# Performance work log

Hardware: AMD Instinct MI355X
Metric: run time of the kernel (lower is better)

## Reference

```python
import jax, jax.numpy as jnp
import numpy as np

DIM = 2048
N_HEADS = 32
N_KV_HEADS = 8
HEAD_DIM = DIM // N_HEADS
B, T = 2, 2048


def setup_inputs() -> dict:
    key = jax.random.key(0)
    ks = jax.random.split(key, 5)
    std = 0.02
    return {
        "x": jax.random.normal(ks[0], (B, T, DIM), dtype=jnp.float32),
        "wq": jax.random.normal(ks[1], (DIM, DIM), dtype=jnp.float32) * std,
        "wk": jax.random.normal(ks[2], (N_KV_HEADS * HEAD_DIM, DIM), dtype=jnp.float32) * std,
        "wv": jax.random.normal(ks[3], (N_KV_HEADS * HEAD_DIM, DIM), dtype=jnp.float32) * std,
        "wo": jax.random.normal(ks[4], (DIM, DIM), dtype=jnp.float32) * std,
    }


def _rope_tables(seq_len, head_dim, dtype):
    inv_freq = 1.0 / (10000.0 ** (jnp.arange(0, head_dim, 2, dtype=jnp.float32) / head_dim))
    t = jnp.arange(seq_len, dtype=jnp.float32)
    freqs = jnp.einsum("i,j->ij", t, inv_freq)          # [T, hd/2]
    emb = jnp.concatenate([freqs, freqs], axis=-1)       # [T, hd]
    return jnp.cos(emb).astype(dtype), jnp.sin(emb).astype(dtype)


def _rotate_half(x):
    h = x.shape[-1] // 2
    return jnp.concatenate([-x[..., h:], x[..., :h]], axis=-1)


def reference(x, wq, wk, wv, wo):
    Bc, Tc, C = x.shape
    q = (x @ wq.T).reshape(Bc, Tc, N_HEADS, HEAD_DIM).transpose(0, 2, 1, 3)      # [B,H,T,hd]
    k = (x @ wk.T).reshape(Bc, Tc, N_KV_HEADS, HEAD_DIM).transpose(0, 2, 1, 3)   # [B,Hk,T,hd]
    v = (x @ wv.T).reshape(Bc, Tc, N_KV_HEADS, HEAD_DIM).transpose(0, 2, 1, 3)

    cos, sin = _rope_tables(Tc, HEAD_DIM, x.dtype)  # [T,hd] broadcast over B,H
    q = q * cos + _rotate_half(q) * sin
    k = k * cos + _rotate_half(k) * sin

    rep = N_HEADS // N_KV_HEADS
    k = jnp.repeat(k, rep, axis=1)  # [B,H,T,hd]
    v = jnp.repeat(v, rep, axis=1)

    scale = 1.0 / np.sqrt(HEAD_DIM)
    scores = jnp.einsum("bhqd,bhkd->bhqk", q, k) * scale   # [B,H,T,T]
    causal = jnp.triu(jnp.ones((Tc, Tc), dtype=bool), k=1)
    scores = jnp.where(causal, jnp.asarray(-jnp.inf, scores.dtype), scores)
    attn = jax.nn.softmax(scores, axis=-1)
    out = jnp.einsum("bhqk,bhkd->bhqd", attn, v)           # [B,H,T,hd]
    out = out.transpose(0, 2, 1, 3).reshape(Bc, Tc, C)
    return out @ wo.T
```

## Files before the change

### kernel.cpp

```cpp
#include <hip/hip_runtime.h>


typedef unsigned short u16;
typedef __attribute__((ext_vector_type(8))) short bf16x8;
typedef __attribute__((ext_vector_type(4))) float f32x4;
typedef __attribute__((ext_vector_type(4))) unsigned short u16x4;

constexpr int T_SEQ = 2048;
constexpr int DIMC  = 2048;
constexpr int NHEAD = 32;
constexpr int HDIM  = 64;
constexpr int KVDIM = 512;
constexpr int BATCH = 2;

__device__ __forceinline__ u16 f2bf(float f) {
    union { float f; unsigned int i; } v; v.f = f;
    unsigned int r = v.i + 0x7FFFu + ((v.i >> 16) & 1u);
    return (u16)(r >> 16);
}

__device__ __forceinline__ unsigned int pack2_bf16(float e0, float e1) {
    return __builtin_amdgcn_perm(__float_as_uint(e1), __float_as_uint(e0),
                                 0x07060302u);
}

typedef __attribute__((address_space(1))) unsigned int as1_uint;
typedef __attribute__((address_space(3))) unsigned int as3_uint;
__device__ __forceinline__ void glds16(const u16* g, u16* l) {
    __builtin_amdgcn_global_load_lds((as1_uint*)(u16*)g, (as3_uint*)l, 16, 0, 0);
}

__global__ __launch_bounds__(256) void cvt5(const float* __restrict__ x,
                                            const float* __restrict__ wq,
                                            const float* __restrict__ wk,
                                            const float* __restrict__ wv,
                                            const float* __restrict__ wo,
                                            u16* __restrict__ xb,  u16* __restrict__ wqb,
                                            u16* __restrict__ wkb, u16* __restrict__ wvb,
                                            u16* __restrict__ wob) {
    constexpr int E0 = BATCH * T_SEQ * DIMC;
    constexpr int E1 = E0 + DIMC * DIMC;
    constexpr int E2 = E1 + KVDIM * DIMC;
    constexpr int E3 = E2 + KVDIM * DIMC;
    constexpr int E4 = E3 + DIMC * DIMC;
    for (int i = (blockIdx.x * 256 + threadIdx.x) * 4; i < E4; i += gridDim.x * 1024) {
        const float* s; u16* d; int off;
        if (i < E0)      { s = x;  d = xb;  off = 0;  }
        else if (i < E1) { s = wq; d = wqb; off = E0; }
        else if (i < E2) { s = wk; d = wkb; off = E1; }
        else if (i < E3) { s = wv; d = wvb; off = E2; }
        else             { s = wo; d = wob; off = E3; }
        f32x4 v = *(const f32x4*)(s + (i - off));
        u16x4 o;
        #pragma unroll
        for (int e = 0; e < 4; ++e) o[e] = f2bf(v[e]);
        *(u16x4*)(d + (i - off)) = o;
    }
}

template <bool OUTF32>
__device__ __forceinline__ void dgemm_core(const u16* __restrict__ A,
                                           const u16* __restrict__ W,
                                           void* __restrict__ Cv,
                                           int rowBase, int colBase,
                                           int N, int K, bool rope) {
    __shared__ __align__(16) u16 Ash[2][128 * 64];
    __shared__ __align__(16) u16 Bsh[2][128 * 64];

    const int tid  = threadIdx.x;
    const int lane = tid & 63;
    const int w    = tid >> 6;
    const int quad = lane >> 4;
    const int ln   = lane & 15;
    const int wm   = (w >> 1) * 64;
    const int wn   = (w & 1) * 64;

    const int sr = lane >> 3;
    const int sc = 8 * ((lane & 7) ^ sr);
    const u16* aS = A + (size_t)(rowBase + w * 8 + sr) * K + sc;
    const u16* bS = W + (size_t)(colBase + w * 8 + sr) * K + sc;

    f32x4 acc[4][4] = {};
    const int NT = K / 64;
    const int swz = (ln & 7) * 8;

    #pragma unroll
    for (int r = 0; r < 4; ++r) {
        glds16(aS + (size_t)(r * 32) * K, &Ash[0][(w + 4 * r) * 512]);
        glds16(bS + (size_t)(r * 32) * K, &Bsh[0][(w + 4 * r) * 512]);
    }

    for (int t = 0; t < NT; ++t) {
        const int cb = t & 1;
        __builtin_amdgcn_s_barrier();
        __builtin_amdgcn_sched_barrier(0);

        if (t + 1 < NT) {
            const size_t ko = (size_t)(t + 1) * 64;
            u16* An = &Ash[cb ^ 1][0];
            u16* Bn = &Bsh[cb ^ 1][0];
            #pragma unroll
            for (int r = 0; r < 4; ++r) {
                glds16(aS + ko + (size_t)(r * 32) * K, An + (w + 4 * r) * 512);
                glds16(bS + ko + (size_t)(r * 32) * K, Bn + (w + 4 * r) * 512);
            }
            __builtin_amdgcn_sched_barrier(0);
            __asm__ __volatile__("s_waitcnt vmcnt(8)" ::: "memory");
        } else {
            __asm__ __volatile__("s_waitcnt vmcnt(0)" ::: "memory");
        }
        __builtin_amdgcn_sched_barrier(0);
        __builtin_amdgcn_s_barrier();

        const u16* Ap = &Ash[cb][0];
        const u16* Bp = &Bsh[cb][0];
        #pragma unroll
        for (int q2 = 0; q2 < 2; ++q2) {
            bf16x8 bwf[4];
            #pragma unroll
            for (int n = 0; n < 4; ++n)
                bwf[n] = *(const bf16x8*)(Bp + (wn + n * 16 + ln) * 64
                                             + ((q2 * 32 + quad * 8) ^ swz));
            __builtin_amdgcn_s_setprio(1);
            #pragma unroll
            for (int m = 0; m < 4; ++m) {
                bf16x8 af = *(const bf16x8*)(Ap + (wm + m * 16 + ln) * 64
                                                + ((q2 * 32 + quad * 8) ^ swz));
                #pragma unroll
                for (int n = 0; n < 4; ++n)
                    acc[m][n] = __builtin_amdgcn_mfma_f32_16x16x32_bf16(af, bwf[n], acc[m][n], 0, 0, 0);
            }
            __builtin_amdgcn_s_setprio(0);
        }
    }

    if (rope) {
        #pragma unroll
        for (int j = 0; j < 2; ++j) {
            const int d = j * 16 + ln;
            const float invrev = exp2f(-(float)d * (13.287712379549449f / 32.0f))
                                 * 0.15915494309189535f;
            #pragma unroll
            for (int i = 0; i < 4; ++i) {
                #pragma unroll
                for (int r = 0; r < 4; ++r) {
                    const int t = (rowBase + wm + i * 16 + quad * 4 + r) & (T_SEQ - 1);
                    float rev = (float)t * invrev;
                    float fr = rev - floorf(rev);
                    float sn = __builtin_amdgcn_sinf(fr);
                    float cs = __builtin_amdgcn_cosf(fr);
                    float a0 = acc[i][j][r], a2 = acc[i][j + 2][r];
                    acc[i][j][r]     = a0 * cs - a2 * sn;
                    acc[i][j + 2][r] = a2 * cs + a0 * sn;
                }
            }
        }
    }

    #pragma unroll
    for (int i = 0; i < 4; ++i) {
        int mrow = rowBase + wm + i * 16 + quad * 4;
        #pragma unroll
        for (int j = 0; j < 4; ++j) {
            int n = colBase + wn + j * 16 + ln;
            #pragma unroll
            for (int r = 0; r < 4; ++r) {
                if constexpr (OUTF32)
                    ((float*)Cv)[(size_t)(mrow + r) * N + n] = acc[i][j][r];
                else
                    ((u16*)Cv)[(size_t)(mrow + r) * N + n] = f2bf(acc[i][j][r]);
            }
        }
    }
}

__global__ __launch_bounds__(256, 2) void qkv_gemm(const u16* __restrict__ xb,
                                                   const u16* __restrict__ wqb,
                                                   const u16* __restrict__ wkb,
                                                   const u16* __restrict__ wvb,
                                                   u16* __restrict__ Qb,
                                                   u16* __restrict__ Kb,
                                                   u16* __restrict__ Vb) {
    const int flat = blockIdx.y * 24 + blockIdx.x;
    const int xcd  = flat & 7;
    const int idx  = flat >> 3;
    const int row  = (xcd >> 2) * 16 + idx / 6;
    const int ct   = (xcd & 3) * 6 + idx % 6;
    const int rowBase = row * 128;

    const u16* W; u16* C; int colBase, N; bool rope;
    if (ct < 16)      { W = wqb; C = Qb; colBase = ct * 128;        N = DIMC;  rope = true; }
    else if (ct < 20) { W = wkb; C = Kb; colBase = (ct - 16) * 128; N = KVDIM; rope = true; }
    else              { W = wvb; C = Vb; colBase = (ct - 20) * 128; N = KVDIM; rope = false; }
    dgemm_core<false>(xb, W, C, rowBase, colBase, N, DIMC, rope);
}

__global__ __launch_bounds__(256, 2) void gemm_out(const u16* __restrict__ A,
                                                   const u16* __restrict__ W,
                                                   float* __restrict__ C) {
    const int flat = blockIdx.y * 16 + blockIdx.x;
    const int xcd  = flat & 7;
    const int idx  = flat >> 3;
    const int row  = (xcd >> 2) * 16 + (idx >> 2);
    const int col  = (xcd & 3) * 4 + (idx & 3);
    dgemm_core<true>(A, W, C, row * 128, col * 128, DIMC, DIMC, false);
}

__global__ __launch_bounds__(256) void transpose_v(const u16* __restrict__ V,
                                                   u16* __restrict__ Vt) {
    __shared__ __align__(16) u16 tile[32][33];
    const int x = threadIdx.x & 31;
    const int y = threadIdx.x >> 5;
    const int tok0 = blockIdx.y * 32;
    const int c0   = blockIdx.x * 32;
    #pragma unroll
    for (int yy = 0; yy < 32; yy += 8)
        tile[y + yy][x] = V[(size_t)(tok0 + y + yy) * KVDIM + c0 + x];
    __syncthreads();
    const int b  = tok0 >> 11;
    const int t0 = tok0 & (T_SEQ - 1);
    #pragma unroll
    for (int yy = 0; yy < 32; yy += 8)
        Vt[(size_t)(b * KVDIM + c0 + y + yy) * T_SEQ + t0 + x] = tile[x][y + yy];
}

__global__ __launch_bounds__(256) void attn(const u16* __restrict__ Q,
                                            const u16* __restrict__ Kx,
                                            const u16* __restrict__ Vt,
                                            u16* __restrict__ O) {
    __shared__ __align__(16) u16 Ks[2][64][72];
    __shared__ __align__(16) u16 Vs[2][64][72];

    const int tid  = threadIdx.x;
    const int lane = tid & 63;
    const int w    = tid >> 6;
    const int quad = lane >> 4;
    const int ln   = lane & 15;
    const int h    = blockIdx.y;
    const int b    = blockIdx.z;
    const int kvh  = h >> 2;

    const int srow = tid >> 2;
    const int c    = tid & 3;
    const int scol = c * 16;
    const int vsb  = 32 * (c >> 1) + 4 * (c & 1);
    const u16* kbase = Kx + (size_t)(b * T_SEQ + srow) * KVDIM + kvh * HDIM + scol;
    const u16* vbase = Vt + (size_t)(b * KVDIM + kvh * HDIM + srow) * T_SEQ;

    const float K1 = 0.125f * 1.4426950408889634f;
    const float K2 = 8.0f * 1.4426950408889634f;

    #pragma unroll
    for (int phase = 0; phase < 2; ++phase) {
        const int qt = phase ? (15 - (int)blockIdx.x) : (int)blockIdx.x;
        const int qr0 = qt * 128 + w * 16;

        const u16* qp0 = Q + (size_t)(b * T_SEQ + qr0 + ln) * DIMC + h * HDIM + quad * 8;
        const u16* qp1 = qp0 + (size_t)64 * DIMC;
        const bf16x8 bq00 = *(const bf16x8*)qp0;
        const bf16x8 bq01 = *(const bf16x8*)(qp0 + 32);
        const bf16x8 bq10 = *(const bf16x8*)qp1;
        const bf16x8 bq11 = *(const bf16x8*)(qp1 + 32);

        f32x4 o0[4] = {}, o1[4] = {};
        float ls0 = 0.0f, ls1 = 0.0f;

        bf16x8 kra = *(const bf16x8*)kbase;
        bf16x8 krb = *(const bf16x8*)(kbase + 8);
        bf16x8 vra = *(const bf16x8*)(vbase + scol);
        bf16x8 vrb = *(const bf16x8*)(vbase + scol + 8);

        const int NTk = 2 * qt + 2;
        for (int kt = 0; kt < NTk; ++kt) {
            const int cb = kt & 1;

            *(bf16x8*)&Ks[cb][srow][scol]     = kra;
            *(bf16x8*)&Ks[cb][srow][scol + 8] = krb;
            {
                union { bf16x8 v; u16x4 h4[2]; } ua, ub;
                ua.v = vra; ub.v = vrb;
                *(u16x4*)&Vs[cb][srow][vsb]      = ua.h4[0];
                *(u16x4*)&Vs[cb][srow][vsb + 8]  = ua.h4[1];
                *(u16x4*)&Vs[cb][srow][vsb + 16] = ub.h4[0];
                *(u16x4*)&Vs[cb][srow][vsb + 24] = ub.h4[1];
            }

            if (kt + 1 < NTk) {
                const size_t ko = (size_t)(kt + 1) * 64;
                kra = *(const bf16x8*)(kbase + ko * KVDIM);
                krb = *(const bf16x8*)(kbase + ko * KVDIM + 8);
                vra = *(const bf16x8*)(vbase + ko + scol);
                vrb = *(const bf16x8*)(vbase + ko + scol + 8);
            }

            __asm__ __volatile__("s_waitcnt lgkmcnt(0)" ::: "memory");
            __builtin_amdgcn_s_barrier();

            f32x4 s0[4], s1[4];
            __builtin_amdgcn_s_setprio(1);
            #pragma unroll
            for (int st = 0; st < 4; ++st) {
                bf16x8 kfa = *(const bf16x8*)&Ks[cb][st * 16 + ln][quad * 8];
                bf16x8 kfb = *(const bf16x8*)&Ks[cb][st * 16 + ln][32 + quad * 8];
                f32x4 z0 = {}, z1 = {};
                s0[st] = __builtin_amdgcn_mfma_f32_16x16x32_bf16(kfa, bq00, z0, 0, 0, 0);
                s1[st] = __builtin_amdgcn_mfma_f32_16x16x32_bf16(kfa, bq10, z1, 0, 0, 0);
                s0[st] = __builtin_amdgcn_mfma_f32_16x16x32_bf16(kfb, bq01, s0[st], 0, 0, 0);
                s1[st] = __builtin_amdgcn_mfma_f32_16x16x32_bf16(kfb, bq11, s1[st], 0, 0, 0);
            }
            __builtin_amdgcn_s_setprio(0);

            unsigned int pk0[8], pk1[8];
            #pragma unroll
            for (int g = 0; g < 2; ++g) {
                const f32x4* s = g ? s1 : s0;
                unsigned int* pk = g ? pk1 : pk0;
                float lsum = 0.0f;
                const int kdiff = kt - (2 * qt + g);
                if (kdiff < 0) {
                    #pragma unroll
                    for (int st = 0; st < 4; ++st) {
                        float e0 = exp2f(fmaf(s[st][0], K1, -K2));
                        float e1 = exp2f(fmaf(s[st][1], K1, -K2));
                        float e2 = exp2f(fmaf(s[st][2], K1, -K2));
                        float e3 = exp2f(fmaf(s[st][3], K1, -K2));
                        lsum += (e0 + e1) + (e2 + e3);
                        pk[2 * st]     = pack2_bf16(e0, e1);
                        pk[2 * st + 1] = pack2_bf16(e2, e3);
                    }
                } else {
                    const int thr = w * 16 + ln - 64 * kdiff;
                    #pragma unroll
                    for (int st = 0; st < 4; ++st) {
                        float e[4];
                        #pragma unroll
                        for (int r = 0; r < 4; ++r) {
                            const int key = st * 16 + quad * 4 + r;
                            e[r] = (key > thr) ? 0.0f : exp2f(fmaf(s[st][r], K1, -K2));
                        }
                        lsum += (e[0] + e[1]) + (e[2] + e[3]);
                        pk[2 * st]     = pack2_bf16(e[0], e[1]);
                        pk[2 * st + 1] = pack2_bf16(e[2], e[3]);
                    }
                }
                if (g) ls1 += lsum; else ls0 += lsum;
            }

            union { unsigned int u[4]; bf16x8 v; } a00, a01, a10, a11;
            a00.u[0] = pk0[0]; a00.u[1] = pk0[1]; a00.u[2] = pk0[2]; a00.u[3] = pk0[3];
            a01.u[0] = pk0[4]; a01.u[1] = pk0[5]; a01.u[2] = pk0[6]; a01.u[3] = pk0[7];
            a10.u[0] = pk1[0]; a10.u[1] = pk1[1]; a10.u[2] = pk1[2]; a10.u[3] = pk1[3];
            a11.u[0] = pk1[4]; a11.u[1] = pk1[5]; a11.u[2] = pk1[6]; a11.u[3] = pk1[7];

            __builtin_amdgcn_s_setprio(1);
            #pragma unroll
            for (int t = 0; t < 4; ++t) {
                bf16x8 vfa = *(const bf16x8*)&Vs[cb][t * 16 + ln][quad * 8];
                bf16x8 vfb = *(const bf16x8*)&Vs[cb][t * 16 + ln][32 + quad * 8];
                o0[t] = __builtin_amdgcn_mfma_f32_16x16x32_bf16(a00.v, vfa, o0[t], 0, 0, 0);
                o1[t] = __builtin_amdgcn_mfma_f32_16x16x32_bf16(a10.v, vfa, o1[t], 0, 0, 0);
                o0[t] = __builtin_amdgcn_mfma_f32_16x16x32_bf16(a01.v, vfb, o0[t], 0, 0, 0);
                o1[t] = __builtin_amdgcn_mfma_f32_16x16x32_bf16(a11.v, vfb, o1[t], 0, 0, 0);
            }
            __builtin_amdgcn_s_setprio(0);
        }

        #pragma unroll
        for (int g = 0; g < 2; ++g) {
            float ls = g ? ls1 : ls0;
            const f32x4* o = g ? o1 : o0;
            ls += __shfl_xor(ls, 16);
            ls += __shfl_xor(ls, 32);
            #pragma unroll
            for (int r = 0; r < 4; ++r) {
                const float inv = 1.0f / __shfl(ls, quad * 4 + r);
                size_t obase = (size_t)(b * T_SEQ + qr0 + g * 64 + quad * 4 + r) * DIMC
                               + h * HDIM;
                #pragma unroll
                for (int t = 0; t < 4; ++t)
                    O[obase + t * 16 + ln] = f2bf(o[t][r] * inv);
            }
        }

        __syncthreads();
    }
}

extern "C" void kernel_launch(void* const* d_in, const int* in_sizes, int n_in,
                              void* d_out, int out_size, void* d_ws, size_t ws_size,
                              hipStream_t stream) {
    const float* x  = (const float*)d_in[0];
    const float* wq = (const float*)d_in[1];
    const float* wk = (const float*)d_in[2];
    const float* wv = (const float*)d_in[3];
    const float* wo = (const float*)d_in[4];
    float* out = (float*)d_out;

    char* ws = (char*)d_ws;
    constexpr size_t MB = 1024 * 1024;
    u16* Qb  = (u16*)(ws);
    u16* Kb  = (u16*)(ws + 16 * MB);
    u16* Vb  = (u16*)(ws + 20 * MB);
    u16* Vtb = (u16*)(ws + 24 * MB);
    u16* AOb = (u16*)(ws + 28 * MB);
    u16* xb  = AOb;
    u16* wqb = (u16*)(ws + 44 * MB);
    u16* wkb = (u16*)(ws + 52 * MB);
    u16* wvb = (u16*)(ws + 54 * MB);
    u16* wob = (u16*)(ws + 56 * MB);
    const int M = BATCH * T_SEQ;

    hipLaunchKernelGGL(cvt5, dim3(2048), dim3(256), 0, stream,
                       x, wq, wk, wv, wo, xb, wqb, wkb, wvb, wob);
    hipLaunchKernelGGL(qkv_gemm, dim3(24, M / 128), dim3(256), 0, stream,
                       xb, wqb, wkb, wvb, Qb, Kb, Vb);
    hipLaunchKernelGGL(transpose_v, dim3(KVDIM / 32, M / 32), dim3(256), 0, stream, Vb, Vtb);
    hipLaunchKernelGGL(attn, dim3(8, NHEAD, BATCH), dim3(256), 0, stream,
                       Qb, Kb, Vtb, AOb);
    hipLaunchKernelGGL(gemm_out, dim3(DIMC / 128, M / 128), dim3(256), 0, stream,
                       AOb, wob, out);
}
```

Measured before the change: 288.9 us.

## Fuse V transpose into attention LDS staging and drop transpose kernel

Removes the separate transpose_v kernel and its global round trip. The attention kernel now loads V row-major (token-major) and transposes it while writing to shared memory, using scalar 16-bit LDS stores at a permuted slot to match the old layout. This saves one kernel launch and about 4 MB of extra global traffic. In exchange, each thread issues 16 scalar LDS stores per tile instead of 4 vector stores, which may cause bank conflicts and more LDS instruction pressure inside the inner loop.

```diff
diff --git a/kernel.cpp b/kernel.cpp
--- a/kernel.cpp
+++ b/kernel.cpp
@@ -206,27 +206,9 @@
     dgemm_core<true>(A, W, C, row * 128, col * 128, DIMC, DIMC, false);
 }
 
-__global__ __launch_bounds__(256) void transpose_v(const u16* __restrict__ V,
-                                                   u16* __restrict__ Vt) {
-    __shared__ __align__(16) u16 tile[32][33];
-    const int x = threadIdx.x & 31;
-    const int y = threadIdx.x >> 5;
-    const int tok0 = blockIdx.y * 32;
-    const int c0   = blockIdx.x * 32;
-    #pragma unroll
-    for (int yy = 0; yy < 32; yy += 8)
-        tile[y + yy][x] = V[(size_t)(tok0 + y + yy) * KVDIM + c0 + x];
-    __syncthreads();
-    const int b  = tok0 >> 11;
-    const int t0 = tok0 & (T_SEQ - 1);
-    #pragma unroll
-    for (int yy = 0; yy < 32; yy += 8)
-        Vt[(size_t)(b * KVDIM + c0 + y + yy) * T_SEQ + t0 + x] = tile[x][y + yy];
-}
-
 __global__ __launch_bounds__(256) void attn(const u16* __restrict__ Q,
                                             const u16* __restrict__ Kx,
-                                            const u16* __restrict__ Vt,
+                                            const u16* __restrict__ Vb,
                                             u16* __restrict__ O) {
     __shared__ __align__(16) u16 Ks[2][64][72];
     __shared__ __align__(16) u16 Vs[2][64][72];
@@ -243,9 +225,11 @@
     const int srow = tid >> 2;
     const int c    = tid & 3;
     const int scol = c * 16;
-    const int vsb  = 32 * (c >> 1) + 4 * (c & 1);
+    const int dc   = c * 16;
+    const int vslot = 32 * (srow >> 5) + 8 * ((srow >> 2) & 3)
+                    + 4 * ((srow >> 4) & 1) + (srow & 3);
     const u16* kbase = Kx + (size_t)(b * T_SEQ + srow) * KVDIM + kvh * HDIM + scol;
-    const u16* vbase = Vt + (size_t)(b * KVDIM + kvh * HDIM + srow) * T_SEQ;
+    const u16* vbase = Vb + (size_t)(b * T_SEQ + srow) * KVDIM + kvh * HDIM + dc;
 
     const float K1 = 0.125f * 1.4426950408889634f;
     const float K2 = 8.0f * 1.4426950408889634f;
@@ -267,8 +251,8 @@
 
         bf16x8 kra = *(const bf16x8*)kbase;
         bf16x8 krb = *(const bf16x8*)(kbase + 8);
-        bf16x8 vra = *(const bf16x8*)(vbase + scol);
-        bf16x8 vrb = *(const bf16x8*)(vbase + scol + 8);
+        bf16x8 vra = *(const bf16x8*)vbase;
+        bf16x8 vrb = *(const bf16x8*)(vbase + 8);
 
         const int NTk = 2 * qt + 2;
         for (int kt = 0; kt < NTk; ++kt) {
@@ -277,20 +261,21 @@
             *(bf16x8*)&Ks[cb][srow][scol]     = kra;
             *(bf16x8*)&Ks[cb][srow][scol + 8] = krb;
             {
-                union { bf16x8 v; u16x4 h4[2]; } ua, ub;
+                union { bf16x8 v; u16 h[8]; } ua, ub;
                 ua.v = vra; ub.v = vrb;
-                *(u16x4*)&Vs[cb][srow][vsb]      = ua.h4[0];
-                *(u16x4*)&Vs[cb][srow][vsb + 8]  = ua.h4[1];
-                *(u16x4*)&Vs[cb][srow][vsb + 16] = ub.h4[0];
-                *(u16x4*)&Vs[cb][srow][vsb + 24] = ub.h4[1];
+                #pragma unroll
+                for (int j = 0; j < 8; ++j) {
+                    Vs[cb][dc + j][vslot]     = ua.h[j];
+                    Vs[cb][dc + 8 + j][vslot] = ub.h[j];
+                }
             }
 
             if (kt + 1 < NTk) {
-                const size_t ko = (size_t)(kt + 1) * 64;
-                kra = *(const bf16x8*)(kbase + ko * KVDIM);
-                krb = *(const bf16x8*)(kbase + ko * KVDIM + 8);
-                vra = *(const bf16x8*)(vbase + ko + scol);
-                vrb = *(const bf16x8*)(vbase + ko + scol + 8);
+                const size_t ko = (size_t)(kt + 1) * 64 * KVDIM;
+                kra = *(const bf16x8*)(kbase + ko);
+                krb = *(const bf16x8*)(kbase + ko + 8);
+                vra = *(const bf16x8*)(vbase + ko);
+                vrb = *(const bf16x8*)(vbase + ko + 8);
             }
 
             __asm__ __volatile__("s_waitcnt lgkmcnt(0)" ::: "memory");
@@ -401,7 +386,6 @@
     u16* Qb  = (u16*)(ws);
     u16* Kb  = (u16*)(ws + 16 * MB);
     u16* Vb  = (u16*)(ws + 20 * MB);
-    u16* Vtb = (u16*)(ws + 24 * MB);
     u16* AOb = (u16*)(ws + 28 * MB);
     u16* xb  = AOb;
     u16* wqb = (u16*)(ws + 44 * MB);
@@ -414,9 +398,8 @@
                        x, wq, wk, wv, wo, xb, wqb, wkb, wvb, wob);
     hipLaunchKernelGGL(qkv_gemm, dim3(24, M / 128), dim3(256), 0, stream,
                        xb, wqb, wkb, wvb, Qb, Kb, Vb);
-    hipLaunchKernelGGL(transpose_v, dim3(KVDIM / 32, M / 32), dim3(256), 0, stream, Vb, Vtb);
     hipLaunchKernelGGL(attn, dim3(8, NHEAD, BATCH), dim3(256), 0, stream,
-                       Qb, Kb, Vtb, AOb);
+                       Qb, Kb, Vb, AOb);
     hipLaunchKernelGGL(gemm_out, dim3(DIMC / 128, M / 128), dim3(256), 0, stream,
                        AOb, wob, out);
 }
```

Measured after the change: 290.4 us. Within noise of the previous version (+0.5%).
